# Kernel optimization log

Hardware: AMD Instinct MI355X
Metric: run time of the kernel (lower is better)

Reference implementation:

```python
import jax, jax.numpy as jnp
import numpy as np
from jax.scipy.stats import norm

H, W = 512, 512
HP, WP = 3, 3            # plane window
T_BINS, R_BINS = 180, 360  # accumulator dims (theta, rho)
THR_VAR = 100.0
ORIGIN = (0, 0)


def setup_inputs() -> dict:
    key = jax.random.key(0)
    k1, _ = jax.random.split(key)
    img = jax.random.uniform(k1, (H, W), dtype=jnp.float32)
    mask = jnp.ones((H, W), dtype=jnp.float32)
    return {"img": img, "mask": mask}


def _shift(img, dx, dy):
    # edge-clamped shifted view, matches xi = clip(hi+dx, 0, H-1)
    ri = jnp.clip(jnp.arange(H) + dx, 0, H - 1)
    ci = jnp.clip(jnp.arange(W) + dy, 0, W - 1)
    return img[ri][:, ci]


def reference(img, mask):
    img = img.astype(jnp.float32)
    dxs = range(-(HP // 2), HP // 2 + 1)
    dys = range(-(WP // 2), WP // 2 + 1)
    sum_x2 = float(sum(dx * dx for dx in dxs) * WP)  # = 6 for 3x3
    sum_y2 = float(sum(dy * dy for dy in dys) * HP)
    n_win = float(HP * WP)

    # ---- local plane fit (vectorized over all pixels, loop over 9 offsets) ----
    alpha = jnp.zeros((H, W), jnp.float32)
    beta = jnp.zeros((H, W), jnp.float32)
    gamma = jnp.zeros((H, W), jnp.float32)
    for dx in dxs:
        for dy in dys:
            s = _shift(img, dx, dy)
            alpha = alpha + dx * s
            beta = beta + dy * s
            gamma = gamma + s
    alpha = alpha / sum_x2 + 1e-6
    beta = beta / sum_y2 + 1e-6
    gamma = gamma / n_win

    # ---- residual variance (faithful to source: uses img[xi, wi]) ----
    eps2 = jnp.zeros((H, W), jnp.float32)
    for dx in dxs:
        row_s = _shift(img, dx, 0)  # img[clip(hi+dx), wi]
        for dy in dys:
            r = row_s - alpha * dy - beta * dx - gamma
            eps2 = eps2 + r * r
    noise_var = eps2 / (n_win - 2.0)
    var_alpha = noise_var / sum_x2
    var_beta = noise_var / sum_y2
    covar_ab = jnp.zeros_like(noise_var)  # sum_xy == 0 for symmetric window

    # ---- polar coordinates + uncertainty propagation ----
    theta = jnp.arctan(beta / alpha)  # in (-pi/2, pi/2)
    xg = (jnp.arange(H, dtype=jnp.float32) - ORIGIN[0])[:, None]
    yg = (jnp.arange(W, dtype=jnp.float32) - ORIGIN[1])[None, :]
    ct, st = jnp.cos(theta), jnp.sin(theta)
    rho = xg * ct + yg * st
    g2 = (alpha * alpha + beta * beta)
    var_theta = (beta * beta * var_alpha + alpha * alpha * var_beta
                 - 2.0 * alpha * beta * covar_ab) / (g2 * g2)
    drho_dt = -xg * st + yg * ct
    var_rho = drho_dt * drho_dt * var_theta

    # ---- Gaussian soft-voting into the accumulator ----
    theta_min, theta_max = -np.pi / 2, np.pi / 2
    rho_max = float(np.sqrt(H ** 2 + W ** 2))
    rho_min = -rho_max
    t_bin = (theta_max - theta_min) / (T_BINS - 1)
    r_bin = (rho_max - rho_min) / (R_BINS - 1)
    # bin i covers [center - bin/2, center + bin/2]
    t_edges = theta_min + (jnp.arange(T_BINS + 1, dtype=jnp.float32) - 0.5) * t_bin
    r_edges = rho_min + (jnp.arange(R_BINS + 1, dtype=jnp.float32) - 0.5) * r_bin

    valid = ((var_theta <= THR_VAR) & (var_rho <= THR_VAR)).astype(jnp.float32) * mask

    P = H * W
    thf = theta.reshape(P)
    rhf = rho.reshape(P)
    sig_t = jnp.sqrt(var_theta + 1e-12).reshape(P)
    sig_r = jnp.sqrt(var_rho + 1e-12).reshape(P)
    vf = valid.reshape(P)

    # per-pixel probability mass in each theta / rho bin (marginal Gaussian CDFs)
    cdf_t = norm.cdf((t_edges[None, :] - thf[:, None]) / sig_t[:, None])  # (P, T+1)
    wt = (cdf_t[:, 1:] - cdf_t[:, :-1]) * vf[:, None]                    # (P, T)
    cdf_r = norm.cdf((r_edges[None, :] - rhf[:, None]) / sig_r[:, None])  # (P, R+1)
    wr = cdf_r[:, 1:] - cdf_r[:, :-1]                                     # (P, R)

    acc = jnp.einsum('pt,pr->tr', wt, wr)  # (T_BINS, R_BINS) accumulated votes
    return acc
```

## Files before the change

### kernel.cpp

```cpp
#include <hip/hip_runtime.h>
#include <math.h>

#define H 512
#define W 512
#define TBINS 180
#define RBINS 360
#define NPIX (H*W)
#define NCELL (TBINS*RBINS)

#define THETA_MIN (-1.5707963267948966f)
#define T_BIN ((float)(3.141592653589793 / 179.0))
#define R_MIN (-724.0773439350246f)
#define R_BIN ((float)(2.0 * 724.0773439350246 / 359.0))
#define THR_VAR 100.0f
#define WSIG 6.0f

#define NT 6
#define KB 256
#define NBLK 1024
#define SCAP 256
#define MPAD 192

typedef short v8s __attribute__((ext_vector_type(8)));
typedef float v4f __attribute__((ext_vector_type(4)));

__device__ __forceinline__ float phi_cdf(float z) {
    return 0.5f * erfcf(-0.70710678118654752f * z);
}
__device__ __forceinline__ unsigned short f2bf(float f) {
    unsigned u = __float_as_uint(f);
    return (unsigned short)((u + 0x7FFF + ((u >> 16) & 1)) >> 16);
}
__device__ __forceinline__ float bf2f(unsigned short b) {
    return __uint_as_float(((unsigned)b) << 16);
}

__global__ void prep_kernel(const float* __restrict__ img,
                            const float* __restrict__ mask,
                            int* __restrict__ cblk,
                            float4* __restrict__ recs,
                            float* __restrict__ mvs) {
    __shared__ int lcnt[NT];
    int tid = threadIdx.x;
    int b = blockIdx.x;
    int gid = b * blockDim.x + tid;
    if (tid < NT) lcnt[tid] = 0;
    __syncthreads();

    int p = gid;
    int hi = p >> 9, wi = p & (W - 1);
    float mv = mask[p];

    int xm = max(hi - 1, 0), xp = min(hi + 1, H - 1);
    int ym = max(wi - 1, 0), yp = min(wi + 1, W - 1);
    const float* r0 = img + xm * W;
    const float* r1 = img + hi * W;
    const float* r2 = img + xp * W;
    float s00 = r0[ym], s01 = r0[wi], s02 = r0[yp];
    float s10 = r1[ym], s11 = r1[wi], s12 = r1[yp];
    float s20 = r2[ym], s21 = r2[wi], s22 = r2[yp];

    float alpha_s = (s20 + s21 + s22) - (s00 + s01 + s02);
    float beta_s  = (s02 + s12 + s22) - (s00 + s10 + s20);
    float gsum    = s00 + s01 + s02 + s10 + s11 + s12 + s20 + s21 + s22;

    float alpha = alpha_s * (1.0f / 6.0f) + 1e-6f;
    float beta  = beta_s  * (1.0f / 6.0f) + 1e-6f;
    float gamma = gsum * (1.0f / 9.0f);

    float cvals[3] = { s01, s11, s21 };
    float eps2 = 0.0f;
    #pragma unroll
    for (int ix = 0; ix < 3; ++ix) {
        float dx = (float)(ix - 1);
        float c = cvals[ix];
        #pragma unroll
        for (int iy = 0; iy < 3; ++iy) {
            float dy = (float)(iy - 1);
            float r = c - alpha * dy - beta * dx - gamma;
            eps2 += r * r;
        }
    }
    float noise_var = eps2 * (1.0f / 7.0f);
    float va = noise_var * (1.0f / 6.0f);
    float g2 = alpha * alpha + beta * beta;
    float var_theta = (beta * beta * va + alpha * alpha * va) / (g2 * g2);

    float x = (float)hi, y = (float)wi;
    float inv_g = rsqrtf(g2);
    float cta = fabsf(alpha) * inv_g;
    float sta = (alpha < 0.0f ? -beta : beta) * inv_g;
    float drho_a = -x * sta + y * cta;
    float var_rho_a = drho_a * drho_a * var_theta;
    bool maybe = (var_theta <= THR_VAR) && (var_rho_a <= THR_VAR * 1.01f) && (mv != 0.0f);

    int myNt[2] = { -1, -1 };
    int myPos[2];
    float4 rc;
    if (maybe) {
        float theta = atanf(beta / alpha);
        float ct = cosf(theta), st = sinf(theta);
        float rho = x * ct + y * st;
        float drho = -x * st + y * ct;
        float var_rho = drho * drho * var_theta;
        if (var_rho <= THR_VAR) {
            float sig_t = sqrtf(var_theta + 1e-12f);
            float sig_r = sqrtf(var_rho + 1e-12f);
            float radr = WSIG * sig_r;
            int rlo = max((int)floorf((rho - radr - R_MIN) / R_BIN - 0.5f), 0);
            int rhi = min((int)ceilf((rho + radr - R_MIN) / R_BIN + 0.5f), RBINS - 1);
            if (rhi >= rlo) {
                rc.x = theta; rc.y = 1.0f / sig_t; rc.z = rho; rc.w = 1.0f / sig_r;
                int nt0 = rlo >> 6, nt1 = rhi >> 6;
                for (int nt = nt0; nt <= nt1; ++nt) {
                    int k = nt - nt0;
                    myNt[k] = nt;
                    myPos[k] = atomicAdd(&lcnt[nt], 1);
                }
            }
        }
    }
    __syncthreads();
    if (tid < NT) cblk[tid * NBLK + b] = lcnt[tid];
    #pragma unroll
    for (int k = 0; k < 2; ++k) {
        if (myNt[k] >= 0) {
            int idx = (myNt[k] * NBLK + b) * SCAP + myPos[k];
            recs[idx] = rc;
            mvs[idx]  = mv;
        }
    }
}

__global__ void __launch_bounds__(512)
gemm_kernel(const float4* __restrict__ recs,
            const float* __restrict__ mvs,
            const int* __restrict__ cblk,
            int* __restrict__ nw,
            float* __restrict__ part) {
    __shared__ __align__(16) unsigned short Ah[MPAD * 32], Al[MPAD * 32];
    __shared__ __align__(16) unsigned short Bh[64 * 32],  Bl[64 * 32];
    __shared__ float4 prec[2][32];
    __shared__ float  pmv[2][32];
    __shared__ int    pref[NBLK];
    __shared__ int    wsum[8], woff[8];

    int nt = blockIdx.x % NT, kb = blockIdx.x / NT;
    int tid = threadIdx.x;
    int lane = tid & 63, wv = tid >> 6;
    int nsub = wv & 3, mhalf = wv >> 2;
    int c0 = nt * 64;
    int nbmax = min(63, RBINS - 1 - c0);

    const int* cb = cblk + nt * NBLK;
    int a0 = cb[2 * tid], a1 = cb[2 * tid + 1];
    int s = a0 + a1;
    #pragma unroll
    for (int d = 1; d < 64; d <<= 1) {
        int u = __shfl_up(s, d);
        if (lane >= d) s += u;
    }
    if (lane == 63) wsum[wv] = s;
    __syncthreads();
    if (tid == 0) {
        int r = 0;
        #pragma unroll
        for (int i = 0; i < 8; ++i) { woff[i] = r; r += wsum[i]; }
    }
    __syncthreads();
    int base = woff[wv] + s;
    pref[2 * tid]     = base - a1;
    pref[2 * tid + 1] = base;
    __syncthreads();

    int cn = pref[NBLK - 1];
    int nck = (cn + 31) >> 5;
    if (kb == 0 && tid == 0) nw[nt] = min(nck, KB);
    if (kb >= nck) return;

    v4f zero = {0.f, 0.f, 0.f, 0.f};
    v4f acc[6];
    #pragma unroll
    for (int i = 0; i < 6; ++i) acc[i] = zero;

    const float4* rb = recs + (size_t)nt * NBLK * SCAP;
    const float*  mb = mvs + (size_t)nt * NBLK * SCAP;

    int pix = tid & 31, g = tid >> 5;

    if (tid < 32) {
        int r = (kb << 5) + tid;
        float4 rcv; rcv.x = 0.f; rcv.y = 0.f; rcv.z = 0.f; rcv.w = 0.f;
        float m = 0.f;
        if (r < min((kb << 5) + 32, cn)) {
            int pos = 0;
            #pragma unroll
            for (int st = 512; st >= 1; st >>= 1)
                if (pos + st <= NBLK && pref[pos + st - 1] <= r) pos += st;
            int off = r - (pos ? pref[pos - 1] : 0);
            int idx = pos * SCAP + off;
            rcv = rb[idx]; m = mb[idx];
        }
        prec[0][tid] = rcv; pmv[0][tid] = m;
    }

    int parity = 0;
    for (int ck = kb; ck < nck; ck += KB, parity ^= 1) {
        __syncthreads();

        bool do_pf = (tid < 32) && (ck + KB < nck);
        float4 pf_rc; pf_rc.x = 0.f; pf_rc.y = 0.f; pf_rc.z = 0.f; pf_rc.w = 0.f;
        float pf_m = 0.f;
        if (do_pf) {
            int r = ((ck + KB) << 5) + tid;
            if (r < min(((ck + KB) << 5) + 32, cn)) {
                int pos = 0;
                #pragma unroll
                for (int st = 512; st >= 1; st >>= 1)
                    if (pos + st <= NBLK && pref[pos + st - 1] <= r) pos += st;
                int off = r - (pos ? pref[pos - 1] : 0);
                int idx = pos * SCAP + off;
                pf_rc = rb[idx]; pf_m = mb[idx];
            }
        }

        {
            float4 rc = prec[parity][pix];
            float m = pmv[parity][pix];
            bool live = (rc.y != 0.0f);
            if (g < 12) {
                int e0 = g << 4;
                float sigt = 1.0f / rc.y;
                int wx = max((int)floorf((rc.x - WSIG * sigt - THETA_MIN) / T_BIN - 0.5f), 0);
                int wy = min((int)ceilf((rc.x + WSIG * sigt - THETA_MIN) / T_BIN + 0.5f), TBINS - 1);
                int sb = e0 * 32 + pix;
                float prev = 0.0f;
                #pragma unroll 1
                for (int i = 0; i <= 16; ++i) {
                    int e = e0 + i;
                    float val;
                    if (!live || e < wx) val = 0.0f;
                    else if (e > wy + 1) val = 1.0f;
                    else {
                        float edge = THETA_MIN + ((float)e - 0.5f) * T_BIN;
                        val = phi_cdf((edge - rc.x) * rc.y);
                    }
                    if (i > 0) {
                        float wt = (val - prev) * m;
                        unsigned short hb = f2bf(wt);
                        Ah[sb + (i - 1) * 32] = hb;
                        Al[sb + (i - 1) * 32] = f2bf(wt - bf2f(hb));
                    }
                    prev = val;
                }
            } else {
                int n0 = (g - 12) << 4;
                float sigr = 1.0f / rc.w;
                int wz = max((int)floorf((rc.z - WSIG * sigr - R_MIN) / R_BIN - 0.5f) - c0, 0);
                int ww = min((int)ceilf((rc.z + WSIG * sigr - R_MIN) / R_BIN + 0.5f) - c0, nbmax);
                int sb = n0 * 32 + pix;
                float prev = 0.0f;
                #pragma unroll 1
                for (int i = 0; i <= 16; ++i) {
                    int n = n0 + i;
                    float val;
                    if (!live || n < wz) val = 0.0f;
                    else if (n > ww + 1) val = 1.0f;
                    else {
                        float edge = R_MIN + ((float)(c0 + n) - 0.5f) * R_BIN;
                        val = phi_cdf((edge - rc.z) * rc.w);
                    }
                    if (i > 0) {
                        float wr = val - prev;
                        unsigned short hb = f2bf(wr);
                        Bh[sb + (i - 1) * 32] = hb;
                        Bl[sb + (i - 1) * 32] = f2bf(wr - bf2f(hb));
                    }
                    prev = val;
                }
            }
        }
        __syncthreads();

        if (do_pf) { prec[parity ^ 1][tid] = pf_rc; pmv[parity ^ 1][tid] = pf_m; }

        int kq = (lane >> 4) * 8;
        int mr = lane & 15;
        v8s bh = *((__shared__ v8s*)&Bh[(nsub * 16 + mr) * 32 + kq]);
        v8s bl = *((__shared__ v8s*)&Bl[(nsub * 16 + mr) * 32 + kq]);
        #pragma unroll
        for (int mt = 0; mt < 6; ++mt) {
            int mbase = (mhalf * 6 + mt) * 16;
            v8s ah = *((__shared__ v8s*)&Ah[(mbase + mr) * 32 + kq]);
            v8s al = *((__shared__ v8s*)&Al[(mbase + mr) * 32 + kq]);
            acc[mt] = __builtin_amdgcn_mfma_f32_16x16x32_bf16(ah, bh, acc[mt], 0, 0, 0);
            acc[mt] = __builtin_amdgcn_mfma_f32_16x16x32_bf16(ah, bl, acc[mt], 0, 0, 0);
            acc[mt] = __builtin_amdgcn_mfma_f32_16x16x32_bf16(al, bh, acc[mt], 0, 0, 0);
        }
    }

    float* slab = part + (size_t)(nt * KB + kb) * (MPAD * 64);
    int col = nsub * 16 + (lane & 15);
    int rq = (lane >> 4) * 4;
    #pragma unroll
    for (int mt = 0; mt < 6; ++mt) {
        int rbase = (mhalf * 6 + mt) * 16 + rq;
        #pragma unroll
        for (int r = 0; r < 4; ++r)
            slab[(rbase + r) * 64 + col] = acc[mt][r];
    }
}

__global__ void __launch_bounds__(1024)
reduce_kernel(const float4* __restrict__ part, const int* __restrict__ nw,
              float4* __restrict__ out) {
    __shared__ float4 sdata[1024];
    int t = blockIdx.x / 45;
    int tid = threadIdx.x;
    int qi = tid & 63, jg = tid >> 6;
    int q = (blockIdx.x % 45) * 64 + qi;
    int n = nw[t];
    const float4* p = part + (size_t)t * KB * (MPAD * 16) + q;
    float4 s; s.x = 0.f; s.y = 0.f; s.z = 0.f; s.w = 0.f;
    #pragma unroll 4
    for (int j = jg; j < n; j += 16) {
        float4 v = p[(size_t)j * (MPAD * 16)];
        s.x += v.x; s.y += v.y; s.z += v.z; s.w += v.w;
    }
    sdata[tid] = s;
    __syncthreads();
    #pragma unroll
    for (int h = 8; h >= 1; h >>= 1) {
        if (jg < h) {
            float4 o = sdata[(jg + h) * 64 + qi];
            s.x += o.x; s.y += o.y; s.z += o.z; s.w += o.w;
            sdata[tid] = s;
        }
        __syncthreads();
    }
    if (jg == 0) {
        int row = q >> 4, c4 = q & 15;
        if (!(t == 5 && c4 >= 10))
            out[row * 90 + t * 16 + c4] = s;
    }
}

extern "C" void kernel_launch(void* const* d_in, const int* in_sizes, int n_in,
                              void* d_out, int out_size, void* d_ws, size_t ws_size,
                              hipStream_t stream) {
    const float* img  = (const float*)d_in[0];
    const float* mask = (const float*)d_in[1];
    float* out = (float*)d_out;

    char* ws = (char*)d_ws;
    size_t off_recs = 32768;
    size_t off_mvs  = off_recs + (size_t)NT * NBLK * SCAP * 16;
    size_t off_nw   = off_mvs + (size_t)NT * NBLK * SCAP * 4;
    size_t off_part = off_nw + 1024;

    int*    cblk = (int*)ws;
    float4* recs = (float4*)(ws + off_recs);
    float*  mvs  = (float*)(ws + off_mvs);
    int*    nw   = (int*)(ws + off_nw);
    float*  part = (float*)(ws + off_part);

    prep_kernel<<<NPIX / 256, 256, 0, stream>>>(img, mask, cblk, recs, mvs);
    gemm_kernel<<<NT * KB, 512, 0, stream>>>(recs, mvs, cblk, nw, part);
    reduce_kernel<<<270, 1024, 0, stream>>>((const float4*)part, nw, (float4*)out);
}
```

Before: 77.76 us.

## Flatten chunks across rho tiles into one global grid-stride work list

The GEMM stage no longer pins each block to one rho tile with a fixed stride over that tile's chunks. Every block now builds the prefix sums for all six tiles, numbers the chunks in one global list, and takes them grid-stride across 512 blocks. Each chunk writes its own partial slab, which the reduce kernel sums over per-tile ranges. This balances uneven per-tile vote counts, at the cost of six-fold redundant prefix work per block, no record prefetch, more partial traffic, and a hard cap of 1024 chunks that would silently drop work if exceeded.

Measured after the change: 81.09 us. +4.3%, slower.

```diff
diff --git a/kernel.cpp b/kernel.cpp
--- a/kernel.cpp
+++ b/kernel.cpp
@@ -6,7 +6,6 @@
 #define TBINS 180
 #define RBINS 360
 #define NPIX (H*W)
-#define NCELL (TBINS*RBINS)
 
 #define THETA_MIN (-1.5707963267948966f)
 #define T_BIN ((float)(3.141592653589793 / 179.0))
@@ -16,10 +15,11 @@
 #define WSIG 6.0f
 
 #define NT 6
-#define KB 256
 #define NBLK 1024
 #define SCAP 256
 #define MPAD 192
+#define GG 512
+#define NCKCAP 1024
 
 typedef short v8s __attribute__((ext_vector_type(8)));
 typedef float v4f __attribute__((ext_vector_type(4)));
@@ -136,97 +136,105 @@
 gemm_kernel(const float4* __restrict__ recs,
             const float* __restrict__ mvs,
             const int* __restrict__ cblk,
-            int* __restrict__ nw,
+            int* __restrict__ ckp_g,
             float* __restrict__ part) {
     __shared__ __align__(16) unsigned short Ah[MPAD * 32], Al[MPAD * 32];
     __shared__ __align__(16) unsigned short Bh[64 * 32],  Bl[64 * 32];
-    __shared__ float4 prec[2][32];
-    __shared__ float  pmv[2][32];
-    __shared__ int    pref[NBLK];
-    __shared__ int    wsum[8], woff[8];
-
-    int nt = blockIdx.x % NT, kb = blockIdx.x / NT;
+    __shared__ float4 prec[32];
+    __shared__ float  pmv[32];
+    __shared__ int    pref[NT][NBLK];
+    __shared__ int    wsum[8][NT], woff[8][NT];
+    __shared__ int    ckp[NT + 1], cnl[NT];
+
     int tid = threadIdx.x;
     int lane = tid & 63, wv = tid >> 6;
     int nsub = wv & 3, mhalf = wv >> 2;
-    int c0 = nt * 64;
-    int nbmax = min(63, RBINS - 1 - c0);
-
-    const int* cb = cblk + nt * NBLK;
-    int a0 = cb[2 * tid], a1 = cb[2 * tid + 1];
-    int s = a0 + a1;
+
+    int a0[NT], a1[NT], s[NT];
+    #pragma unroll
+    for (int t = 0; t < NT; ++t) {
+        a0[t] = cblk[t * NBLK + 2 * tid];
+        a1[t] = cblk[t * NBLK + 2 * tid + 1];
+        s[t] = a0[t] + a1[t];
+    }
     #pragma unroll
     for (int d = 1; d < 64; d <<= 1) {
-        int u = __shfl_up(s, d);
-        if (lane >= d) s += u;
-    }
-    if (lane == 63) wsum[wv] = s;
+        #pragma unroll
+        for (int t = 0; t < NT; ++t) {
+            int u = __shfl_up(s[t], d);
+            if (lane >= d) s[t] += u;
+        }
+    }
+    if (lane == 63) {
+        #pragma unroll
+        for (int t = 0; t < NT; ++t) wsum[wv][t] = s[t];
+    }
+    __syncthreads();
+    if (tid == 0) {
+        #pragma unroll
+        for (int t = 0; t < NT; ++t) {
+            int r = 0;
+            #pragma unroll
+            for (int i = 0; i < 8; ++i) { woff[i][t] = r; r += wsum[i][t]; }
+        }
+    }
+    __syncthreads();
+    #pragma unroll
+    for (int t = 0; t < NT; ++t) {
+        int base = woff[wv][t] + s[t];
+        pref[t][2 * tid]     = base - a1[t];
+        pref[t][2 * tid + 1] = base;
+    }
     __syncthreads();
     if (tid == 0) {
         int r = 0;
         #pragma unroll
-        for (int i = 0; i < 8; ++i) { woff[i] = r; r += wsum[i]; }
-    }
-    __syncthreads();
-    int base = woff[wv] + s;
-    pref[2 * tid]     = base - a1;
-    pref[2 * tid + 1] = base;
-    __syncthreads();
-
-    int cn = pref[NBLK - 1];
-    int nck = (cn + 31) >> 5;
-    if (kb == 0 && tid == 0) nw[nt] = min(nck, KB);
-    if (kb >= nck) return;
-
-    v4f zero = {0.f, 0.f, 0.f, 0.f};
-    v4f acc[6];
-    #pragma unroll
-    for (int i = 0; i < 6; ++i) acc[i] = zero;
-
-    const float4* rb = recs + (size_t)nt * NBLK * SCAP;
-    const float*  mb = mvs + (size_t)nt * NBLK * SCAP;
+        for (int t = 0; t < NT; ++t) {
+            ckp[t] = min(r, NCKCAP);
+            int cn = pref[t][NBLK - 1];
+            cnl[t] = cn;
+            r += (cn + 31) >> 5;
+        }
+        ckp[NT] = min(r, NCKCAP);
+    }
+    __syncthreads();
+    if (blockIdx.x == 0 && tid <= NT) ckp_g[tid] = ckp[tid];
+    int nchunks = ckp[NT];
 
     int pix = tid & 31, g = tid >> 5;
 
-    if (tid < 32) {
-        int r = (kb << 5) + tid;
-        float4 rcv; rcv.x = 0.f; rcv.y = 0.f; rcv.z = 0.f; rcv.w = 0.f;
-        float m = 0.f;
-        if (r < min((kb << 5) + 32, cn)) {
-            int pos = 0;
-            #pragma unroll
-            for (int st = 512; st >= 1; st >>= 1)
-                if (pos + st <= NBLK && pref[pos + st - 1] <= r) pos += st;
-            int off = r - (pos ? pref[pos - 1] : 0);
-            int idx = pos * SCAP + off;
-            rcv = rb[idx]; m = mb[idx];
-        }
-        prec[0][tid] = rcv; pmv[0][tid] = m;
-    }
-
-    int parity = 0;
-    for (int ck = kb; ck < nck; ck += KB, parity ^= 1) {
-        __syncthreads();
-
-        bool do_pf = (tid < 32) && (ck + KB < nck);
-        float4 pf_rc; pf_rc.x = 0.f; pf_rc.y = 0.f; pf_rc.z = 0.f; pf_rc.w = 0.f;
-        float pf_m = 0.f;
-        if (do_pf) {
-            int r = ((ck + KB) << 5) + tid;
-            if (r < min(((ck + KB) << 5) + 32, cn)) {
+    for (int c = blockIdx.x; c < nchunks; c += GG) {
+        if (c != (int)blockIdx.x) __syncthreads();
+
+        int t = 0;
+        #pragma unroll
+        for (int i = 1; i < NT; ++i) if (c >= ckp[i]) t = i;
+        int c0 = t * 64;
+        int nbmax = min(63, RBINS - 1 - c0);
+        int cn = cnl[t];
+        int k0 = (c - ckp[t]) << 5;
+        int k1 = min(k0 + 32, cn);
+
+        if (tid < 32) {
+            int r = k0 + tid;
+            float4 rcv; rcv.x = 0.f; rcv.y = 0.f; rcv.z = 0.f; rcv.w = 0.f;
+            float m = 0.f;
+            if (r < k1) {
                 int pos = 0;
                 #pragma unroll
                 for (int st = 512; st >= 1; st >>= 1)
-                    if (pos + st <= NBLK && pref[pos + st - 1] <= r) pos += st;
-                int off = r - (pos ? pref[pos - 1] : 0);
-                int idx = pos * SCAP + off;
-                pf_rc = rb[idx]; pf_m = mb[idx];
+                    if (pos + st <= NBLK && pref[t][pos + st - 1] <= r) pos += st;
+                int off = r - (pos ? pref[t][pos - 1] : 0);
+                int idx = (t * NBLK + pos) * SCAP + off;
+                rcv = recs[idx]; m = mvs[idx];
             }
-        }
+            prec[tid] = rcv; pmv[tid] = m;
+        }
+        __syncthreads();
 
         {
-            float4 rc = prec[parity][pix];
-            float m = pmv[parity][pix];
+            float4 rc = prec[pix];
+            float m = pmv[pix];
             bool live = (rc.y != 0.0f);
             if (g < 12) {
                 int e0 = g << 4;
@@ -282,7 +290,10 @@
         }
         __syncthreads();
 
-        if (do_pf) { prec[parity ^ 1][tid] = pf_rc; pmv[parity ^ 1][tid] = pf_m; }
+        v4f zero = {0.f, 0.f, 0.f, 0.f};
+        v4f acc[6];
+        #pragma unroll
+        for (int i = 0; i < 6; ++i) acc[i] = zero;
 
         int kq = (lane >> 4) * 8;
         int mr = lane & 15;
@@ -297,34 +308,33 @@
             acc[mt] = __builtin_amdgcn_mfma_f32_16x16x32_bf16(ah, bl, acc[mt], 0, 0, 0);
             acc[mt] = __builtin_amdgcn_mfma_f32_16x16x32_bf16(al, bh, acc[mt], 0, 0, 0);
         }
-    }
-
-    float* slab = part + (size_t)(nt * KB + kb) * (MPAD * 64);
-    int col = nsub * 16 + (lane & 15);
-    int rq = (lane >> 4) * 4;
-    #pragma unroll
-    for (int mt = 0; mt < 6; ++mt) {
-        int rbase = (mhalf * 6 + mt) * 16 + rq;
-        #pragma unroll
-        for (int r = 0; r < 4; ++r)
-            slab[(rbase + r) * 64 + col] = acc[mt][r];
+
+        float* slab = part + (size_t)c * (MPAD * 64);
+        int col = nsub * 16 + (lane & 15);
+        int rq = (lane >> 4) * 4;
+        #pragma unroll
+        for (int mt = 0; mt < 6; ++mt) {
+            int rbase = (mhalf * 6 + mt) * 16 + rq;
+            #pragma unroll
+            for (int r = 0; r < 4; ++r)
+                slab[(rbase + r) * 64 + col] = acc[mt][r];
+        }
     }
 }
 
 __global__ void __launch_bounds__(1024)
-reduce_kernel(const float4* __restrict__ part, const int* __restrict__ nw,
+reduce_kernel(const float4* __restrict__ part, const int* __restrict__ ckp_g,
               float4* __restrict__ out) {
     __shared__ float4 sdata[1024];
     int t = blockIdx.x / 45;
     int tid = threadIdx.x;
     int qi = tid & 63, jg = tid >> 6;
     int q = (blockIdx.x % 45) * 64 + qi;
-    int n = nw[t];
-    const float4* p = part + (size_t)t * KB * (MPAD * 16) + q;
+    int n0 = ckp_g[t], n1 = ckp_g[t + 1];
     float4 s; s.x = 0.f; s.y = 0.f; s.z = 0.f; s.w = 0.f;
     #pragma unroll 4
-    for (int j = jg; j < n; j += 16) {
-        float4 v = p[(size_t)j * (MPAD * 16)];
+    for (int j = n0 + jg; j < n1; j += 16) {
+        float4 v = part[(size_t)j * (MPAD * 16) + q];
         s.x += v.x; s.y += v.y; s.z += v.z; s.w += v.w;
     }
     sdata[tid] = s;
@@ -350,21 +360,21 @@
                               hipStream_t stream) {
     const float* img  = (const float*)d_in[0];
     const float* mask = (const float*)d_in[1];
-    float* out = (float*)d_out;
+    float4* out = (float4*)d_out;
 
     char* ws = (char*)d_ws;
     size_t off_recs = 32768;
     size_t off_mvs  = off_recs + (size_t)NT * NBLK * SCAP * 16;
-    size_t off_nw   = off_mvs + (size_t)NT * NBLK * SCAP * 4;
-    size_t off_part = off_nw + 1024;
+    size_t off_ckp  = off_mvs + (size_t)NT * NBLK * SCAP * 4;
+    size_t off_part = off_ckp + 1024;
 
     int*    cblk = (int*)ws;
     float4* recs = (float4*)(ws + off_recs);
     float*  mvs  = (float*)(ws + off_mvs);
-    int*    nw   = (int*)(ws + off_nw);
+    int*    ckp  = (int*)(ws + off_ckp);
     float*  part = (float*)(ws + off_part);
 
     prep_kernel<<<NPIX / 256, 256, 0, stream>>>(img, mask, cblk, recs, mvs);
-    gemm_kernel<<<NT * KB, 512, 0, stream>>>(recs, mvs, cblk, nw, part);
-    reduce_kernel<<<270, 1024, 0, stream>>>((const float4*)part, nw, (float4*)out);
-}
+    gemm_kernel<<<GG, 512, 0, stream>>>(recs, mvs, cblk, ckp, part);
+    reduce_kernel<<<270, 1024, 0, stream>>>((const float4*)part, ckp, (float4*)out);
+}
```
